# Performance work log

Measured on AMD Instinct MI355X. Metric: run time of the kernel, lower is better.

The kernel has to match this reference:

```python
import jax, jax.numpy as jnp
import numpy as np

B, T, D_IN, EMB, H = 2, 2048, 1024, 1024, 16
HD = EMB // H  # head_dim = 64


def setup_inputs() -> dict:
    key = jax.random.key(0)
    ks = jax.random.split(key, 3)
    scale_qkv = 1.0 / np.sqrt(D_IN)
    scale_o = 1.0 / np.sqrt(EMB)
    return {
        "x": jax.random.normal(ks[0], (B, T, D_IN), dtype=jnp.float32),
        "W_qkv": jax.random.normal(ks[1], (D_IN, 3 * EMB), dtype=jnp.float32) * scale_qkv,
        "b_qkv": jnp.zeros((3 * EMB,), dtype=jnp.float32),
        "W_o": jax.random.normal(ks[2], (EMB, EMB), dtype=jnp.float32) * scale_o,
        "b_o": jnp.zeros((EMB,), dtype=jnp.float32),
    }


def reference(x, W_qkv, b_qkv, W_o, b_o):
    b, t, _ = x.shape
    qkv = x @ W_qkv + b_qkv                      # [B,T,3*EMB]
    # Match torch: reshape to (B,T,H,3*HD) -> permute -> chunk into q,k,v
    qkv = qkv.reshape(b, t, H, 3 * HD).transpose(0, 2, 1, 3)  # [B,H,T,3*HD]
    q, k, v = jnp.split(qkv, 3, axis=-1)         # each [B,H,T,HD]
    scale = 1.0 / jnp.sqrt(jnp.asarray(HD, dtype=q.dtype))
    scores = jnp.einsum("bhqd,bhkd->bhqk", q, k) * scale  # [B,H,T,T]
    attn = jax.nn.softmax(scores, axis=-1)
    values = jnp.einsum("bhqk,bhkd->bhqd", attn, v)       # [B,H,T,HD]
    values = values.transpose(0, 2, 1, 3).reshape(b, t, EMB)
    return values @ W_o + b_o
```

## Files before the change

### kernel.cpp

```cpp
#include <hip/hip_runtime.h>
#include <math.h>

typedef __bf16 bf16x8 __attribute__((ext_vector_type(8)));
typedef float f32x4 __attribute__((ext_vector_type(4)));

#define GPTR(p) ((const __attribute__((address_space(1))) void*)(p))
#define LPTR(p) ((__attribute__((address_space(3))) void*)(p))

#define QSCALE 0.18033688011112042f

__device__ __forceinline__ unsigned short f2bf(float f) {
  unsigned int u = __float_as_uint(f);
  u += 0x7FFFu + ((u >> 16) & 1u);
  return (unsigned short)(u >> 16);
}

__device__ __forceinline__ unsigned int pack_bf2(float lo, float hi) {
  return __builtin_amdgcn_perm(__float_as_uint(hi) + 0x8000u,
                               __float_as_uint(lo) + 0x8000u, 0x07060302u);
}

__device__ __forceinline__ float fast_exp2(float x) {
#if __has_builtin(__builtin_amdgcn_exp2f)
  return __builtin_amdgcn_exp2f(x);
#else
  return exp2f(x);
#endif
}

__device__ __forceinline__ f32x4 zero4() {
  f32x4 z; z[0] = 0.f; z[1] = 0.f; z[2] = 0.f; z[3] = 0.f; return z;
}

__global__ void conv_x_bf16(const float* __restrict__ in, unsigned short* __restrict__ out) {
  int i = (blockIdx.x * 256 + threadIdx.x) * 4;
  float4 v = *(const float4*)(in + i);
  ushort4 o;
  o.x = f2bf(v.x); o.y = f2bf(v.y); o.z = f2bf(v.z); o.w = f2bf(v.w);
  *(ushort4*)(out + i) = o;
}

__global__ void transpose_conv(const float* __restrict__ in, unsigned short* __restrict__ out,
                               int K, int N) {
  __shared__ float tile[64][65];
  int k0 = blockIdx.y * 64, n0 = blockIdx.x * 64;
  int t = threadIdx.x;
#pragma unroll
  for (int p = 0; p < 16; ++p) {
    int l = p * 256 + t; int r = l >> 6, c = l & 63;
    tile[r][c] = in[(size_t)(k0 + r) * N + n0 + c];
  }
  __syncthreads();
#pragma unroll
  for (int p = 0; p < 16; ++p) {
    int l = p * 256 + t; int r = l >> 6, c = l & 63;
    out[(size_t)(n0 + r) * K + k0 + c] = f2bf(tile[c][r]);
  }
}

__global__ __launch_bounds__(256) void gemm_qkv(
    const unsigned short* __restrict__ A, const unsigned short* __restrict__ Bt,
    const float* __restrict__ bias,
    unsigned short* __restrict__ Qd, unsigned short* __restrict__ Kd,
    unsigned short* __restrict__ Vtd) {
  __shared__ unsigned short As[128 * 32];
  __shared__ unsigned short Bs[128 * 32];
  const int tid = threadIdx.x, wave = tid >> 6, lane = tid & 63;
  const int quad = lane >> 4, l16 = lane & 15;
  const int wm = (wave >> 1) * 64, wn = (wave & 1) * 64;
  const int m0 = blockIdx.y * 128, n0 = blockIdx.x * 128;
  f32x4 acc[4][4];
#pragma unroll
  for (int i = 0; i < 4; ++i)
#pragma unroll
    for (int j = 0; j < 4; ++j) acc[i][j] = zero4();

  const int c = wave * 64 + lane;
  const int rA = c >> 2, o16 = (c & 3) * 8;

  for (int k0 = 0; k0 < 1024; k0 += 32) {
    __syncthreads();
    __builtin_amdgcn_global_load_lds(GPTR(A + (size_t)(m0 + rA) * 1024 + k0 + o16),
                                     LPTR(As + wave * 512), 16, 0, 0);
    __builtin_amdgcn_global_load_lds(GPTR(A + (size_t)(m0 + 64 + rA) * 1024 + k0 + o16),
                                     LPTR(As + 2048 + wave * 512), 16, 0, 0);
    __builtin_amdgcn_global_load_lds(GPTR(Bt + (size_t)(n0 + rA) * 1024 + k0 + o16),
                                     LPTR(Bs + wave * 512), 16, 0, 0);
    __builtin_amdgcn_global_load_lds(GPTR(Bt + (size_t)(n0 + 64 + rA) * 1024 + k0 + o16),
                                     LPTR(Bs + 2048 + wave * 512), 16, 0, 0);
    __syncthreads();
    bf16x8 af[4], bfr[4];
#pragma unroll
    for (int mt = 0; mt < 4; ++mt)
      af[mt] = *(const bf16x8*)(As + (wm + mt * 16 + l16) * 32 + quad * 8);
#pragma unroll
    for (int nt = 0; nt < 4; ++nt)
      bfr[nt] = *(const bf16x8*)(Bs + (wn + nt * 16 + l16) * 32 + quad * 8);
#pragma unroll
    for (int mt = 0; mt < 4; ++mt)
#pragma unroll
      for (int nt = 0; nt < 4; ++nt)
        acc[mt][nt] = __builtin_amdgcn_mfma_f32_16x16x32_bf16(af[mt], bfr[nt], acc[mt][nt], 0, 0, 0);
  }

#pragma unroll
  for (int mt = 0; mt < 4; ++mt) {
#pragma unroll
    for (int nt = 0; nt < 4; ++nt) {
      int m = m0 + wm + mt * 16 + quad * 4;
      int n = n0 + wn + nt * 16 + l16;
      float bv = bias[n];
      int h = n / 192, rem = n - h * 192;
      int which = rem >> 6, d = rem & 63;
      int b = m >> 11, t0 = m & 2047;
      size_t head = (size_t)(b * 16 + h);
      f32x4 a = acc[mt][nt];
      if (which == 0) {
        size_t base = (head * 2048 + t0) * 64 + d;
#pragma unroll
        for (int i = 0; i < 4; ++i)
          Qd[base + (size_t)i * 64] = f2bf((a[i] + bv) * QSCALE);
      } else if (which == 1) {
        size_t base = head * 131072 + (size_t)(t0 >> 6) * 4096;
#pragma unroll
        for (int i = 0; i < 4; ++i) {
          int tt = t0 + i;
          Kd[base + (tt & 63) * 64 + (((d >> 3) ^ (tt & 7)) << 3) + (d & 7)] = f2bf(a[i] + bv);
        }
      } else {
        size_t base = head * 131072 + (size_t)(t0 >> 6) * 4096;
        ushort4 o;
        o.x = f2bf(a[0] + bv); o.y = f2bf(a[1] + bv);
        o.z = f2bf(a[2] + bv); o.w = f2bf(a[3] + bv);
        *(ushort4*)(Vtd + base + d * 64 + (((((t0 & 63) >> 3)) ^ (d & 7)) << 3) + (t0 & 7)) = o;
      }
    }
  }
}

__global__ __launch_bounds__(256) void flash_attn(
    const unsigned short* __restrict__ Qg,
    const unsigned short* __restrict__ Kg,
    const unsigned short* __restrict__ Vg,
    unsigned short* __restrict__ att) {
  __shared__ unsigned short Ks[4096];
  __shared__ unsigned short Vs[4096];
  __shared__ unsigned short Ps[8192];
  const int tid = threadIdx.x, wave = tid >> 6, lane = tid & 63;
  const int quad = lane >> 4, l16 = lane & 15;
  const int h7 = l16 & 7;
  const int bh = blockIdx.y;
  const int q0 = blockIdx.x * 128 + wave * 32;

  bf16x8 bq[2][2];
#pragma unroll
  for (int qg = 0; qg < 2; ++qg)
#pragma unroll
    for (int kh = 0; kh < 2; ++kh)
      bq[qg][kh] = *(const bf16x8*)(Qg + ((size_t)bh * 2048 + q0 + qg * 16 + l16) * 64 + kh * 32 + quad * 8);

  f32x4 o[2][4];
#pragma unroll
  for (int qg = 0; qg < 2; ++qg)
#pragma unroll
    for (int i = 0; i < 4; ++i) o[qg][i] = zero4();
  float l_run[2] = {0.f, 0.f};

  unsigned short* pb = Ps + wave * 2048;
  const unsigned short* Kt = Kg + (size_t)bh * 131072;
  const unsigned short* Vt = Vg + (size_t)bh * 131072;

  for (int tile = 0; tile < 32; ++tile) {
    __syncthreads();
    const unsigned short* Kb = Kt + tile * 4096 + lane * 8;
    const unsigned short* Vb = Vt + tile * 4096 + lane * 8;
    __builtin_amdgcn_global_load_lds(GPTR(Kb + wave * 512),       LPTR(Ks + wave * 512), 16, 0, 0);
    __builtin_amdgcn_global_load_lds(GPTR(Kb + (4 + wave) * 512), LPTR(Ks + (4 + wave) * 512), 16, 0, 0);
    __builtin_amdgcn_global_load_lds(GPTR(Vb + wave * 512),       LPTR(Vs + wave * 512), 16, 0, 0);
    __builtin_amdgcn_global_load_lds(GPTR(Vb + (4 + wave) * 512), LPTR(Vs + (4 + wave) * 512), 16, 0, 0);
    __syncthreads();

    f32x4 s[2][4];
#pragma unroll
    for (int qg = 0; qg < 2; ++qg)
#pragma unroll
      for (int kt = 0; kt < 4; ++kt) s[qg][kt] = zero4();
#pragma unroll
    for (int kt = 0; kt < 4; ++kt) {
#pragma unroll
      for (int kh = 0; kh < 2; ++kh) {
        bf16x8 a = *(const bf16x8*)(Ks + (kt * 16 + l16) * 64 + (((kh * 4 + quad) ^ h7) << 3));
        s[0][kt] = __builtin_amdgcn_mfma_f32_16x16x32_bf16(a, bq[0][kh], s[0][kt], 0, 0, 0);
        s[1][kt] = __builtin_amdgcn_mfma_f32_16x16x32_bf16(a, bq[1][kh], s[1][kt], 0, 0, 0);
      }
    }

#pragma unroll
    for (int qg = 0; qg < 2; ++qg) {
      int qrow = qg * 16 + l16;
      float lsum = 0.f;
      float pv[4][4];
#pragma unroll
      for (int kt = 0; kt < 4; ++kt)
#pragma unroll
        for (int r = 0; r < 4; ++r) {
          float p = fast_exp2(s[qg][kt][r]);
          pv[kt][r] = p;
          lsum += p;
        }
#pragma unroll
      for (int kt = 0; kt < 4; ++kt) {
        uint2 pk;
        pk.x = pack_bf2(pv[kt][0], pv[kt][1]);
        pk.y = pack_bf2(pv[kt][2], pv[kt][3]);
        *(uint2*)(pb + qrow * 64 + (((2 * kt + (quad >> 1)) ^ h7) << 3) + (quad & 1) * 4) = pk;
      }
      lsum += __shfl_xor(lsum, 16);
      lsum += __shfl_xor(lsum, 32);
      l_run[qg] += lsum;
    }

#pragma unroll
    for (int st = 0; st < 2; ++st) {
      bf16x8 pf0 = *(const bf16x8*)(pb + (l16) * 64 + (((st * 4 + quad) ^ h7) << 3));
      bf16x8 pf1 = *(const bf16x8*)(pb + (16 + l16) * 64 + (((st * 4 + quad) ^ h7) << 3));
#pragma unroll
      for (int mt = 0; mt < 4; ++mt) {
        bf16x8 av = *(const bf16x8*)(Vs + (mt * 16 + l16) * 64 + (((st * 4 + quad) ^ h7) << 3));
        o[0][mt] = __builtin_amdgcn_mfma_f32_16x16x32_bf16(av, pf0, o[0][mt], 0, 0, 0);
        o[1][mt] = __builtin_amdgcn_mfma_f32_16x16x32_bf16(av, pf1, o[1][mt], 0, 0, 0);
      }
    }
  }

  int b = bh >> 4, h = bh & 15;
#pragma unroll
  for (int qg = 0; qg < 2; ++qg) {
    float inv_l = 1.f / l_run[qg];
    unsigned short* orow = att + ((size_t)b * 2048 + q0 + qg * 16 + l16) * 1024 + h * 64;
#pragma unroll
    for (int mt = 0; mt < 4; ++mt) {
      ushort4 ov;
      ov.x = f2bf(o[qg][mt][0] * inv_l);
      ov.y = f2bf(o[qg][mt][1] * inv_l);
      ov.z = f2bf(o[qg][mt][2] * inv_l);
      ov.w = f2bf(o[qg][mt][3] * inv_l);
      *(ushort4*)(orow + mt * 16 + quad * 4) = ov;
    }
  }
}

__global__ __launch_bounds__(256) void gemm_out(
    const unsigned short* __restrict__ A, const unsigned short* __restrict__ Bt,
    const float* __restrict__ bias, float* __restrict__ out) {
  __shared__ unsigned short As[128 * 32];
  __shared__ unsigned short Bs[128 * 32];
  const int tid = threadIdx.x, wave = tid >> 6, lane = tid & 63;
  const int quad = lane >> 4, l16 = lane & 15;
  const int wm = (wave >> 1) * 64, wn = (wave & 1) * 64;
  const int m0 = blockIdx.y * 128, n0 = blockIdx.x * 128;
  f32x4 acc[4][4];
#pragma unroll
  for (int i = 0; i < 4; ++i)
#pragma unroll
    for (int j = 0; j < 4; ++j) acc[i][j] = zero4();

  const int c = wave * 64 + lane;
  const int rA = c >> 2, o16 = (c & 3) * 8;

  for (int k0 = 0; k0 < 1024; k0 += 32) {
    __syncthreads();
    __builtin_amdgcn_global_load_lds(GPTR(A + (size_t)(m0 + rA) * 1024 + k0 + o16),
                                     LPTR(As + wave * 512), 16, 0, 0);
    __builtin_amdgcn_global_load_lds(GPTR(A + (size_t)(m0 + 64 + rA) * 1024 + k0 + o16),
                                     LPTR(As + 2048 + wave * 512), 16, 0, 0);
    __builtin_amdgcn_global_load_lds(GPTR(Bt + (size_t)(n0 + rA) * 1024 + k0 + o16),
                                     LPTR(Bs + wave * 512), 16, 0, 0);
    __builtin_amdgcn_global_load_lds(GPTR(Bt + (size_t)(n0 + 64 + rA) * 1024 + k0 + o16),
                                     LPTR(Bs + 2048 + wave * 512), 16, 0, 0);
    __syncthreads();
    bf16x8 af[4], bfr[4];
#pragma unroll
    for (int mt = 0; mt < 4; ++mt)
      af[mt] = *(const bf16x8*)(As + (wm + mt * 16 + l16) * 32 + quad * 8);
#pragma unroll
    for (int nt = 0; nt < 4; ++nt)
      bfr[nt] = *(const bf16x8*)(Bs + (wn + nt * 16 + l16) * 32 + quad * 8);
#pragma unroll
    for (int mt = 0; mt < 4; ++mt)
#pragma unroll
      for (int nt = 0; nt < 4; ++nt)
        acc[mt][nt] = __builtin_amdgcn_mfma_f32_16x16x32_bf16(af[mt], bfr[nt], acc[mt][nt], 0, 0, 0);
  }

#pragma unroll
  for (int mt = 0; mt < 4; ++mt) {
#pragma unroll
    for (int nt = 0; nt < 4; ++nt) {
      int m = m0 + wm + mt * 16 + quad * 4;
      int n = n0 + wn + nt * 16 + l16;
      float bv = bias[n];
      float* orow = out + (size_t)m * 1024 + n;
      orow[0]        = acc[mt][nt][0] + bv;
      orow[1024]     = acc[mt][nt][1] + bv;
      orow[2 * 1024] = acc[mt][nt][2] + bv;
      orow[3 * 1024] = acc[mt][nt][3] + bv;
    }
  }
}

extern "C" void kernel_launch(void* const* d_in, const int* in_sizes, int n_in,
                              void* d_out, int out_size, void* d_ws, size_t ws_size,
                              hipStream_t stream) {
  const float* x    = (const float*)d_in[0];
  const float* Wqkv = (const float*)d_in[1];
  const float* bqkv = (const float*)d_in[2];
  const float* Wo   = (const float*)d_in[3];
  const float* bo   = (const float*)d_in[4];
  float* out = (float*)d_out;

  unsigned short* xb    = (unsigned short*)d_ws;
  unsigned short* wqkvt = xb    + (size_t)4096 * 1024;
  unsigned short* wot   = wqkvt + (size_t)3072 * 1024;
  unsigned short* Qd    = wot   + (size_t)1024 * 1024;
  unsigned short* Kd    = Qd    + (size_t)32 * 2048 * 64;
  unsigned short* Vtd   = Kd    + (size_t)32 * 2048 * 64;
  unsigned short* attb  = Vtd   + (size_t)32 * 2048 * 64;

  conv_x_bf16<<<4096, 256, 0, stream>>>(x, xb);
  transpose_conv<<<dim3(48, 16), 256, 0, stream>>>(Wqkv, wqkvt, 1024, 3072);
  transpose_conv<<<dim3(16, 16), 256, 0, stream>>>(Wo, wot, 1024, 1024);
  gemm_qkv<<<dim3(24, 32), 256, 0, stream>>>(xb, wqkvt, bqkv, Qd, Kd, Vtd);
  flash_attn<<<dim3(16, 32), 256, 0, stream>>>(Qd, Kd, Vtd, attb);
  gemm_out<<<dim3(8, 32), 256, 0, stream>>>(attb, wot, bo, out);
}
```

Before: 222.1 us.

## Split attention keys across wave pairs and keep P in registers

Each pair of waves now shares 64 query rows and splits every 64-key tile in half. The waves combine their partial outputs and row sums through LDS at the end. P is no longer written to LDS and read back. It is packed straight into 16x16x16 MFMA B operands using the accumulator layout. This removes the per-tile LDS round trip for P. The cost is a larger register footprint (16 output accumulators and 8 Q fragments per wave) and an end-of-kernel reduction.

```diff
diff --git a/kernel.cpp b/kernel.cpp
--- a/kernel.cpp
+++ b/kernel.cpp
@@ -3,6 +3,7 @@
 
 typedef __bf16 bf16x8 __attribute__((ext_vector_type(8)));
 typedef float f32x4 __attribute__((ext_vector_type(4)));
+typedef short s16x4 __attribute__((ext_vector_type(4)));
 
 #define GPTR(p) ((const __attribute__((address_space(1))) void*)(p))
 #define LPTR(p) ((__attribute__((address_space(3))) void*)(p))
@@ -143,30 +144,32 @@
     const unsigned short* __restrict__ Kg,
     const unsigned short* __restrict__ Vg,
     unsigned short* __restrict__ att) {
-  __shared__ unsigned short Ks[4096];
-  __shared__ unsigned short Vs[4096];
-  __shared__ unsigned short Ps[8192];
+  __shared__ __align__(16) char smem[33792];
+  unsigned short* Ks = (unsigned short*)smem;
+  unsigned short* Vs = Ks + 4096;
+  float* redO = (float*)smem;
+  float* redL = (float*)(smem + 32768);
   const int tid = threadIdx.x, wave = tid >> 6, lane = tid & 63;
   const int quad = lane >> 4, l16 = lane & 15;
   const int h7 = l16 & 7;
+  const int qhalf = wave >> 1, kh2 = wave & 1;
   const int bh = blockIdx.y;
-  const int q0 = blockIdx.x * 128 + wave * 32;
-
-  bf16x8 bq[2][2];
-#pragma unroll
-  for (int qg = 0; qg < 2; ++qg)
+  const int q0 = blockIdx.x * 128 + qhalf * 64;
+
+  bf16x8 bq[4][2];
+#pragma unroll
+  for (int qg = 0; qg < 4; ++qg)
 #pragma unroll
     for (int kh = 0; kh < 2; ++kh)
       bq[qg][kh] = *(const bf16x8*)(Qg + ((size_t)bh * 2048 + q0 + qg * 16 + l16) * 64 + kh * 32 + quad * 8);
 
-  f32x4 o[2][4];
-#pragma unroll
-  for (int qg = 0; qg < 2; ++qg)
-#pragma unroll
-    for (int i = 0; i < 4; ++i) o[qg][i] = zero4();
-  float l_run[2] = {0.f, 0.f};
-
-  unsigned short* pb = Ps + wave * 2048;
+  f32x4 o[4][4];
+#pragma unroll
+  for (int mt = 0; mt < 4; ++mt)
+#pragma unroll
+    for (int qg = 0; qg < 4; ++qg) o[mt][qg] = zero4();
+  float lacc[4] = {0.f, 0.f, 0.f, 0.f};
+
   const unsigned short* Kt = Kg + (size_t)bh * 131072;
   const unsigned short* Vt = Vg + (size_t)bh * 131072;
 
@@ -180,72 +183,89 @@
     __builtin_amdgcn_global_load_lds(GPTR(Vb + (4 + wave) * 512), LPTR(Vs + (4 + wave) * 512), 16, 0, 0);
     __syncthreads();
 
-    f32x4 s[2][4];
-#pragma unroll
-    for (int qg = 0; qg < 2; ++qg)
-#pragma unroll
-      for (int kt = 0; kt < 4; ++kt) s[qg][kt] = zero4();
-#pragma unroll
-    for (int kt = 0; kt < 4; ++kt) {
+    f32x4 s[4][2];
+#pragma unroll
+    for (int qg = 0; qg < 4; ++qg)
+#pragma unroll
+      for (int kt = 0; kt < 2; ++kt) s[qg][kt] = zero4();
+#pragma unroll
+    for (int kt = 0; kt < 2; ++kt) {
+      int krow = kh2 * 32 + kt * 16 + l16;
 #pragma unroll
       for (int kh = 0; kh < 2; ++kh) {
-        bf16x8 a = *(const bf16x8*)(Ks + (kt * 16 + l16) * 64 + (((kh * 4 + quad) ^ h7) << 3));
-        s[0][kt] = __builtin_amdgcn_mfma_f32_16x16x32_bf16(a, bq[0][kh], s[0][kt], 0, 0, 0);
-        s[1][kt] = __builtin_amdgcn_mfma_f32_16x16x32_bf16(a, bq[1][kh], s[1][kt], 0, 0, 0);
-      }
-    }
-
-#pragma unroll
-    for (int qg = 0; qg < 2; ++qg) {
-      int qrow = qg * 16 + l16;
-      float lsum = 0.f;
-      float pv[4][4];
-#pragma unroll
-      for (int kt = 0; kt < 4; ++kt)
-#pragma unroll
-        for (int r = 0; r < 4; ++r) {
-          float p = fast_exp2(s[qg][kt][r]);
-          pv[kt][r] = p;
-          lsum += p;
-        }
-#pragma unroll
-      for (int kt = 0; kt < 4; ++kt) {
-        uint2 pk;
-        pk.x = pack_bf2(pv[kt][0], pv[kt][1]);
-        pk.y = pack_bf2(pv[kt][2], pv[kt][3]);
-        *(uint2*)(pb + qrow * 64 + (((2 * kt + (quad >> 1)) ^ h7) << 3) + (quad & 1) * 4) = pk;
-      }
-      lsum += __shfl_xor(lsum, 16);
-      lsum += __shfl_xor(lsum, 32);
-      l_run[qg] += lsum;
-    }
-
-#pragma unroll
-    for (int st = 0; st < 2; ++st) {
-      bf16x8 pf0 = *(const bf16x8*)(pb + (l16) * 64 + (((st * 4 + quad) ^ h7) << 3));
-      bf16x8 pf1 = *(const bf16x8*)(pb + (16 + l16) * 64 + (((st * 4 + quad) ^ h7) << 3));
+        bf16x8 a = *(const bf16x8*)(Ks + krow * 64 + (((kh * 4 + quad) ^ h7) << 3));
+#pragma unroll
+        for (int qg = 0; qg < 4; ++qg)
+          s[qg][kt] = __builtin_amdgcn_mfma_f32_16x16x32_bf16(a, bq[qg][kh], s[qg][kt], 0, 0, 0);
+      }
+    }
+
+#pragma unroll
+    for (int kt = 0; kt < 2; ++kt) {
+      s16x4 pB[4];
+#pragma unroll
+      for (int qg = 0; qg < 4; ++qg) {
+        float p0 = fast_exp2(s[qg][kt][0]);
+        float p1 = fast_exp2(s[qg][kt][1]);
+        float p2 = fast_exp2(s[qg][kt][2]);
+        float p3 = fast_exp2(s[qg][kt][3]);
+        lacc[qg] += (p0 + p1) + (p2 + p3);
+        union { unsigned int u[2]; s16x4 v; } pk;
+        pk.u[0] = pack_bf2(p0, p1);
+        pk.u[1] = pack_bf2(p2, p3);
+        pB[qg] = pk.v;
+      }
+      int cV = kh2 * 4 + kt * 2 + (quad >> 1);
 #pragma unroll
       for (int mt = 0; mt < 4; ++mt) {
-        bf16x8 av = *(const bf16x8*)(Vs + (mt * 16 + l16) * 64 + (((st * 4 + quad) ^ h7) << 3));
-        o[0][mt] = __builtin_amdgcn_mfma_f32_16x16x32_bf16(av, pf0, o[0][mt], 0, 0, 0);
-        o[1][mt] = __builtin_amdgcn_mfma_f32_16x16x32_bf16(av, pf1, o[1][mt], 0, 0, 0);
-      }
-    }
-  }
-
-  int b = bh >> 4, h = bh & 15;
-#pragma unroll
-  for (int qg = 0; qg < 2; ++qg) {
-    float inv_l = 1.f / l_run[qg];
-    unsigned short* orow = att + ((size_t)b * 2048 + q0 + qg * 16 + l16) * 1024 + h * 64;
-#pragma unroll
-    for (int mt = 0; mt < 4; ++mt) {
-      ushort4 ov;
-      ov.x = f2bf(o[qg][mt][0] * inv_l);
-      ov.y = f2bf(o[qg][mt][1] * inv_l);
-      ov.z = f2bf(o[qg][mt][2] * inv_l);
-      ov.w = f2bf(o[qg][mt][3] * inv_l);
-      *(ushort4*)(orow + mt * 16 + quad * 4) = ov;
+        s16x4 aV = *(const s16x4*)(Vs + (mt * 16 + l16) * 64 + ((cV ^ h7) << 3) + (quad & 1) * 4);
+#pragma unroll
+        for (int qg = 0; qg < 4; ++qg)
+          o[mt][qg] = __builtin_amdgcn_mfma_f32_16x16x16bf16_1k(aV, pB[qg], o[mt][qg], 0, 0, 0);
+      }
+    }
+  }
+
+  float lfull[4];
+#pragma unroll
+  for (int qg = 0; qg < 4; ++qg) {
+    float lw = lacc[qg];
+    lw += __shfl_xor(lw, 16);
+    lw += __shfl_xor(lw, 32);
+    lfull[qg] = lw;
+  }
+  __syncthreads();
+  if (kh2 == 1) {
+    float* ob = redO + qhalf * 4096;
+#pragma unroll
+    for (int mt = 0; mt < 4; ++mt)
+#pragma unroll
+      for (int qg = 0; qg < 4; ++qg)
+        *(f32x4*)(ob + ((qg * 4 + mt) * 4 + quad) * 64 + l16 * 4) = o[mt][qg];
+    if (quad == 0) {
+#pragma unroll
+      for (int qg = 0; qg < 4; ++qg)
+        redL[qhalf * 64 + qg * 16 + l16] = lfull[qg];
+    }
+  }
+  __syncthreads();
+  if (kh2 == 0) {
+    int b = bh >> 4, h = bh & 15;
+    float* ob = redO + qhalf * 4096;
+#pragma unroll
+    for (int qg = 0; qg < 4; ++qg) {
+      float linv = 1.f / (lfull[qg] + redL[qhalf * 64 + qg * 16 + l16]);
+      unsigned short* orow = att + ((size_t)b * 2048 + q0 + qg * 16 + l16) * 1024 + h * 64;
+#pragma unroll
+      for (int mt = 0; mt < 4; ++mt) {
+        f32x4 part = *(const f32x4*)(ob + ((qg * 4 + mt) * 4 + quad) * 64 + l16 * 4);
+        ushort4 ov;
+        ov.x = f2bf((o[mt][qg][0] + part[0]) * linv);
+        ov.y = f2bf((o[mt][qg][1] + part[1]) * linv);
+        ov.z = f2bf((o[mt][qg][2] + part[2]) * linv);
+        ov.w = f2bf((o[mt][qg][3] + part[3]) * linv);
+        *(ushort4*)(orow + mt * 16 + quad * 4) = ov;
+      }
     }
   }
 }
```

After: 222.5 us. No clear change (+0.2%).
